# Performance work log

Hardware: AMD Instinct MI355X
Metric: run time of the kernel (lower is better)

Reference implementation:

```python
import jax, jax.numpy as jnp
import numpy as np

B, S, H, NH = 2, 2048, 1024, 16
HD = H // NH  # head_dim = 64


def setup_inputs() -> dict:
    key = jax.random.key(0)
    k1, k2, k3, k4, k5 = jax.random.split(key, 5)
    hidden_states = jax.random.normal(k1, (B, S, H), dtype=jnp.float32)
    # additive causal mask: 0 on/below diagonal, -1e9 above
    causal = jnp.tril(jnp.ones((S, S), dtype=jnp.bool_))
    attention_mask = jnp.where(causal, 0.0, -1e9).astype(jnp.float32)[None, None, :, :]
    scale = 0.02
    Wq = jax.random.normal(k2, (H, H), dtype=jnp.float32) * scale
    Wk = jax.random.normal(k3, (H, H), dtype=jnp.float32) * scale
    Wv = jax.random.normal(k4, (H, H), dtype=jnp.float32) * scale
    Wo = jax.random.normal(k5, (H, H), dtype=jnp.float32) * scale
    return {"hidden_states": hidden_states, "attention_mask": attention_mask,
            "Wq": Wq, "Wk": Wk, "Wv": Wv, "Wo": Wo}


def reference(hidden_states, attention_mask, Wq, Wk, Wv, Wo):
    b, s, _ = hidden_states.shape
    # nn.Linear: y = x @ W.T
    q = (hidden_states @ Wq.T).reshape(b, s, NH, HD).transpose(0, 2, 1, 3)  # [B,NH,S,HD]
    k = (hidden_states @ Wk.T).reshape(b, s, NH, HD).transpose(0, 2, 1, 3)
    v = (hidden_states @ Wv.T).reshape(b, s, NH, HD).transpose(0, 2, 1, 3)
    scores = jnp.einsum('bhqd,bhkd->bhqk', q, k) / jnp.sqrt(jnp.float32(HD))
    scores = scores + attention_mask
    attn = jax.nn.softmax(scores, axis=-1)
    out = jnp.einsum('bhqk,bhkd->bhqd', attn, v)  # [B,NH,S,HD]
    out = out.transpose(0, 2, 1, 3).reshape(b, s, H)
    return out @ Wo.T
```

## Files before the change

### kernel.cpp

```cpp
#include <hip/hip_runtime.h>
#include <hip/hip_bf16.h>

#define B_   2
#define S_   2048
#define H_   1024
#define NH_  16
#define HD_  64
#define MTOT 4096
#define KD   1024

typedef __attribute__((ext_vector_type(4)))  float    f32x4;
typedef __attribute__((ext_vector_type(16))) float    f32x16;
typedef __attribute__((ext_vector_type(8)))  short    bf16x8;
typedef __attribute__((ext_vector_type(4)))  short    bf16x4;
typedef __attribute__((ext_vector_type(2)))  unsigned u32x2;
typedef __attribute__((ext_vector_type(4)))  unsigned u32x4;

__device__ inline short f2bf(float x) {
    union { float f; unsigned u; } v; v.f = x;
    unsigned r = v.u + 0x7fffu + ((v.u >> 16) & 1u);
    return (short)(r >> 16);
}
__device__ inline unsigned pk2(float lo, float hi) {
    return (unsigned)(unsigned short)f2bf(lo) | ((unsigned)(unsigned short)f2bf(hi) << 16);
}
__device__ inline unsigned cvtpk(float lo, float hi) {
    unsigned r;
    asm("v_cvt_pk_bf16_f32 %0, %1, %2" : "=v"(r) : "v"(lo), "v"(hi));
    return r;
}
__device__ inline float max3f(float a, float b, float c) {
    float r;
    asm("v_max3_f32 %0, %1, %2, %3" : "=v"(r) : "v"(a), "v"(b), "v"(c));
    return r;
}
__device__ inline void gload16(const void* g, void* l) {
    __builtin_amdgcn_global_load_lds(
        (const __attribute__((address_space(1))) unsigned*)g,
        (__attribute__((address_space(3))) unsigned*)l, 16, 0, 0);
}

__global__ __launch_bounds__(256) void cvt_x(const float* __restrict__ x,
                                             unsigned* __restrict__ xb) {
    const size_t i = ((size_t)blockIdx.x * 256 + threadIdx.x) * 8;
    const f32x4 a = *(const f32x4*)(x + i);
    const f32x4 b = *(const f32x4*)(x + i + 4);
    u32x4 p;
    p[0] = pk2(a[0], a[1]); p[1] = pk2(a[2], a[3]);
    p[2] = pk2(b[0], b[1]); p[3] = pk2(b[2], b[3]);
    *(u32x4*)(xb + i / 2) = p;
}

__global__ __launch_bounds__(256) void wcvt(const float* __restrict__ W0,
                                            const float* __restrict__ W1,
                                            const float* __restrict__ W2,
                                            const float* __restrict__ W3,
                                            unsigned* __restrict__ wb) {
    const float* W = (blockIdx.y == 0) ? W0 : (blockIdx.y == 1) ? W1
                   : (blockIdx.y == 2) ? W2 : W3;
    const size_t i = ((size_t)blockIdx.x * 256 + threadIdx.x) * 8;
    const f32x4 a = *(const f32x4*)(W + i);
    const f32x4 b = *(const f32x4*)(W + i + 4);
    u32x4 p;
    p[0] = pk2(a[0], a[1]); p[1] = pk2(a[2], a[3]);
    p[2] = pk2(b[0], b[1]); p[3] = pk2(b[2], b[3]);
    *(u32x4*)(wb + (size_t)blockIdx.y * (H_ * KD / 2) + i / 2) = p;
}

template <int MODE>
__global__ __launch_bounds__(256) void gemm_m97(const short* __restrict__ A,
                                                const short* __restrict__ Wb,
                                                short* __restrict__ outb,
                                                float* __restrict__ outf) {
    __shared__ short Sm[128 * 128];
    short* As = Sm;
    short* Bs = Sm + 8192;

    const int tid = threadIdx.x, wave = tid >> 6, lane = tid & 63;
    const int wm = (wave >> 1) * 64, wn = (wave & 1) * 64;
    const int m0 = blockIdx.x * 128;

    int n0, widx;
    if constexpr (MODE == 0) {
        widx = blockIdx.y >> 3;
        n0 = (blockIdx.y & 7) * 128;
    } else {
        widx = 0;
        n0 = blockIdx.y * 128;
    }
    const short* W = Wb + (size_t)widx * H_ * KD;

    f32x4 acc[4][4] = {};

    for (int k0 = 0; k0 < KD; k0 += 64) {
#pragma unroll
        for (int c = 0; c < 4; ++c) {
            const int lin = wave * 4096 + c * 1024 + lane * 16;
            const int row = lin >> 7;
            const int col = (lin & 127) ^ ((row & 7) << 4);
            gload16(A + (size_t)(m0 + row) * KD + k0 + (col >> 1),
                    (char*)As + wave * 4096 + c * 1024);
            gload16(W + (size_t)(n0 + row) * KD + k0 + (col >> 1),
                    (char*)Bs + wave * 4096 + c * 1024);
        }
        __syncthreads();

#pragma unroll
        for (int ks = 0; ks < 2; ++ks) {
            bf16x8 af[4], bf[4];
#pragma unroll
            for (int i = 0; i < 4; ++i) {
                const int row = wm + i * 16 + (lane & 15);
                af[i] = *(const bf16x8*)((char*)As + row * 128 +
                        ((ks * 64 + (lane >> 4) * 16) ^ ((row & 7) << 4)));
            }
#pragma unroll
            for (int j = 0; j < 4; ++j) {
                const int row = wn + j * 16 + (lane & 15);
                bf[j] = *(const bf16x8*)((char*)Bs + row * 128 +
                        ((ks * 64 + (lane >> 4) * 16) ^ ((row & 7) << 4)));
            }
#pragma unroll
            for (int i = 0; i < 4; ++i)
#pragma unroll
                for (int j = 0; j < 4; ++j)
                    acc[i][j] = __builtin_amdgcn_mfma_f32_16x16x32_bf16(af[i], bf[j], acc[i][j], 0, 0, 0);
        }
        __syncthreads();
    }

    if constexpr (MODE == 0) {
        if (widx == 2) {
#pragma unroll
            for (int i = 0; i < 4; ++i)
#pragma unroll
                for (int j = 0; j < 4; ++j) {
                    const int m = m0 + wm + i * 16 + (lane >> 4) * 4;
                    const int n = n0 + wn + j * 16 + (lane & 15);
                    const int bb = m >> 11, s = m & 2047;
                    const int hd = n >> 6, d = n & 63;
                    bf16x4 w;
#pragma unroll
                    for (int r = 0; r < 4; ++r) w[r] = f2bf(acc[i][j][r]);
                    *(bf16x4*)(outb + (size_t)2 * MTOT * H_ +
                               (((size_t)(bb * NH_ + hd)) * HD_ + d) * S_ + s) = w;
                }
        } else {
#pragma unroll
            for (int i = 0; i < 4; ++i)
#pragma unroll
                for (int j = 0; j < 4; ++j)
#pragma unroll
                    for (int r = 0; r < 4; ++r) {
                        const int mi = wm + i * 16 + (lane >> 4) * 4 + r;
                        const int ni = wn + j * 16 + (lane & 15);
                        const int byt = (mi * 256 + ni * 2) ^ ((mi & 7) << 4);
                        *(short*)((char*)Sm + byt) = f2bf(acc[i][j][r]);
                    }
            __syncthreads();
            const int row = tid >> 1, half = tid & 1;
            const int m = m0 + row, bb = m >> 11, s = m & 2047;
            const int hh = (n0 >> 6) + half;
            short* dst = outb + (size_t)widx * MTOT * H_ +
                         (((size_t)(bb * NH_ + hh)) * S_ + s) * HD_;
#pragma unroll
            for (int k = 0; k < 8; ++k) {
                const int byt = (row * 256 + half * 128 + k * 16) ^ ((row & 7) << 4);
                *(bf16x8*)(dst + k * 8) = *(const bf16x8*)((char*)Sm + byt);
            }
        }
    } else {
#pragma unroll
        for (int i = 0; i < 4; ++i)
#pragma unroll
            for (int j = 0; j < 4; ++j)
#pragma unroll
                for (int r = 0; r < 4; ++r) {
                    const int m = m0 + wm + i * 16 + (lane >> 4) * 4 + r;
                    const int n = n0 + wn + j * 16 + (lane & 15);
                    outf[(size_t)m * H_ + n] = acc[i][j][r];
                }
    }
}

__global__ __launch_bounds__(256, 3) void flash5(const short* __restrict__ Qb,
                                                 const short* __restrict__ Kb,
                                                 const short* __restrict__ Vtb,
                                                 short* __restrict__ Ob) {
    const int bx = blockIdx.x;
    const int hi = bx >> 8, u = bx & 255;
    const int h = u >> 4, tq = u & 15;
    const int qt = hi ? (15 - tq) : tq;
    const int b  = hi;

    const int tid = threadIdx.x, qg = tid >> 6, lane = tid & 63;
    const int q0 = qt * 128;
    const int qw0 = q0 + qg * 32;
    const size_t hoff = ((size_t)(b * NH_ + h)) * S_ * HD_;
    const short* Q  = Qb  + hoff;
    const short* K  = Kb  + hoff;
    const short* Vt = Vtb + hoff;

    const int ql = lane & 31;
    const int hh = lane >> 5;

    bf16x8 qf[4];
#pragma unroll
    for (int ds = 0; ds < 4; ++ds)
        qf[ds] = *(const bf16x8*)(Q + (size_t)(qw0 + ql) * HD_ + ds * 16 + hh * 8);

    f32x16 ot[2] = {};
    float mrun = -1e30f, lrun = 0.f;
    const float c2 = 0.18033688011112042f;

    const int niter = (qw0 + 95) >> 6;
    for (int kt = 0; kt < niter; ++kt) {
        bf16x8 kf[2][4];
#pragma unroll
        for (int t = 0; t < 2; ++t)
#pragma unroll
            for (int ds = 0; ds < 4; ++ds)
                kf[t][ds] = *(const bf16x8*)(K + (size_t)(kt * 64 + t * 32 + ql) * HD_ +
                                             ds * 16 + hh * 8);

        f32x16 st[2] = {};
        __builtin_amdgcn_s_setprio(1);
#pragma unroll
        for (int t = 0; t < 2; ++t)
#pragma unroll
            for (int ds = 0; ds < 4; ++ds)
                st[t] = __builtin_amdgcn_mfma_f32_32x32x16_bf16(kf[t][ds], qf[ds], st[t], 0, 0, 0);
        __builtin_amdgcn_s_setprio(0);

        bf16x8 vf[2][4];
#pragma unroll
        for (int dt = 0; dt < 2; ++dt)
#pragma unroll
            for (int ks = 0; ks < 4; ++ks)
                vf[dt][ks] = *(const bf16x8*)(Vt + (size_t)(dt * 32 + ql) * S_ +
                                              kt * 64 + ks * 16 + hh * 8);

        const bool need_mask = (kt * 64 + 63) > qw0;
        float sraw[32];
#pragma unroll
        for (int t = 0; t < 2; ++t)
#pragma unroll
            for (int r = 0; r < 16; ++r) {
                float v = st[t][r];
                if (need_mask) {
                    const int key = kt * 64 + t * 32 + (r & 3) + 8 * (r >> 2) + 4 * hh;
                    if (key > qw0 + ql) v = -1e30f;
                }
                sraw[t * 16 + r] = v;
            }

        float ma = fmaxf(sraw[0], sraw[1]);
        float mb = fmaxf(sraw[2], sraw[3]);
#pragma unroll
        for (int i = 4; i < 32; i += 4) {
            ma = max3f(ma, sraw[i],     sraw[i + 1]);
            mb = max3f(mb, sraw[i + 2], sraw[i + 3]);
        }
        const float pmax = fmaxf(fmaxf(ma, mb), __shfl_xor(fmaxf(ma, mb), 32, 64));

        if (!__all((pmax - mrun) <= 44.36f)) {
            const float mnew = fmaxf(mrun, pmax);
            const float corr = exp2f((mrun - mnew) * c2);
            mrun = mnew;
            lrun *= corr;
#pragma unroll
            for (int dt = 0; dt < 2; ++dt)
#pragma unroll
                for (int r = 0; r < 16; ++r) ot[dt][r] *= corr;
        }
        const float mc = mrun * c2;

        float p[32];
#pragma unroll
        for (int i = 0; i < 32; ++i) p[i] = exp2f(fmaf(sraw[i], c2, -mc));
        float ts[16];
#pragma unroll
        for (int i = 0; i < 16; ++i) ts[i] = p[i] + p[i + 16];
#pragma unroll
        for (int stp = 8; stp >= 1; stp >>= 1)
#pragma unroll
            for (int i = 0; i < 8; ++i)
                if (i < stp) ts[i] += ts[i + stp];
        lrun += ts[0] + __shfl_xor(ts[0], 32, 64);

#pragma unroll
        for (int ks = 0; ks < 4; ++ks) {
            const int t = ks >> 1, rb = (ks & 1) * 8;
            const unsigned a0 = cvtpk(p[t * 16 + rb + 0], p[t * 16 + rb + 1]);
            const unsigned a1 = cvtpk(p[t * 16 + rb + 2], p[t * 16 + rb + 3]);
            const unsigned a2 = cvtpk(p[t * 16 + rb + 4], p[t * 16 + rb + 5]);
            const unsigned a3 = cvtpk(p[t * 16 + rb + 6], p[t * 16 + rb + 7]);
            const unsigned s0 = __shfl_xor(a0, 32, 64);
            const unsigned s1 = __shfl_xor(a1, 32, 64);
            const unsigned s2 = __shfl_xor(a2, 32, 64);
            const unsigned s3 = __shfl_xor(a3, 32, 64);
            u32x4 pw;
            pw[0] = hh ? s2 : a0;
            pw[1] = hh ? s3 : a1;
            pw[2] = hh ? a2 : s0;
            pw[3] = hh ? a3 : s1;
            const bf16x8 pf = __builtin_bit_cast(bf16x8, pw);
            __builtin_amdgcn_s_setprio(1);
#pragma unroll
            for (int dt = 0; dt < 2; ++dt)
                ot[dt] = __builtin_amdgcn_mfma_f32_32x32x16_bf16(vf[dt][ks], pf, ot[dt], 0, 0, 0);
            __builtin_amdgcn_s_setprio(0);
        }
    }

    const float inv = 1.f / lrun;
    short* orow = Ob + ((size_t)(b * S_) + q0 + qg * 32 + ql) * H_ + h * HD_;
#pragma unroll
    for (int dt = 0; dt < 2; ++dt)
#pragma unroll
        for (int g4 = 0; g4 < 4; ++g4) {
            const int dbase = dt * 32 + 8 * g4 + 4 * hh;
            u32x2 w;
            w[0] = cvtpk(ot[dt][g4 * 4 + 0] * inv, ot[dt][g4 * 4 + 1] * inv);
            w[1] = cvtpk(ot[dt][g4 * 4 + 2] * inv, ot[dt][g4 * 4 + 3] * inv);
            *(u32x2*)(orow + dbase) = w;
        }
}

extern "C" void kernel_launch(void* const* d_in, const int* in_sizes, int n_in,
                              void* d_out, int out_size, void* d_ws, size_t ws_size,
                              hipStream_t stream) {
    const float* x  = (const float*)d_in[0];
    const float* Wq = (const float*)d_in[2];
    const float* Wk = (const float*)d_in[3];
    const float* Wv = (const float*)d_in[4];
    const float* Wo = (const float*)d_in[5];
    float* out = (float*)d_out;

    short* qkv = (short*)d_ws;
    short* xb  = qkv + (size_t)3 * MTOT * H_;
    short* wb  = xb + (size_t)MTOT * H_;

    cvt_x<<<2048, 256, 0, stream>>>(x, (unsigned*)xb);
    wcvt<<<dim3(512, 4), 256, 0, stream>>>(Wq, Wk, Wv, Wo, (unsigned*)wb);

    gemm_m97<0><<<dim3(32, 24), 256, 0, stream>>>(xb, wb, qkv, nullptr);

    flash5<<<dim3(512), 256, 0, stream>>>(
        qkv, qkv + (size_t)MTOT * H_, qkv + (size_t)2 * MTOT * H_, xb);

    gemm_m97<1><<<dim3(32, 8), 256, 0, stream>>>(
        xb, wb + (size_t)3 * H_ * KD, nullptr, out);
}
```

Measured before the change: 148.5 us.

## Split KV loop across wave pairs in flash kernel, stage V-transpose stores via LDS

Restructures the flash attention kernel so each wave handles 64 query rows (two 32-row halves sharing K/V fragment loads), and pairs of waves split the key tiles by parity, merging partial softmax states through shared memory at the end. Block-to-(batch, head, query-tile) mapping is changed to pair causal-complementary query tiles within a block and to group heads, for load balance and L2 locality. Separately, the V-transpose epilogue of the QKV GEMM now goes through swizzled LDS to emit 16-byte coalesced stores instead of scattered 8-byte writes. The cost is higher register pressure (launch bounds lowered to 2 blocks per SM), extra LDS, and a final merge step.

```diff
diff --git a/kernel.cpp b/kernel.cpp
--- a/kernel.cpp
+++ b/kernel.cpp
@@ -135,16 +135,24 @@
             for (int i = 0; i < 4; ++i)
 #pragma unroll
                 for (int j = 0; j < 4; ++j) {
-                    const int m = m0 + wm + i * 16 + (lane >> 4) * 4;
-                    const int n = n0 + wn + j * 16 + (lane & 15);
-                    const int bb = m >> 11, s = m & 2047;
-                    const int hd = n >> 6, d = n & 63;
+                    const int mi2 = (wm + i * 16 + (lane >> 4) * 4) * 2;
+                    const int ni  = wn + j * 16 + (lane & 15);
                     bf16x4 w;
 #pragma unroll
                     for (int r = 0; r < 4; ++r) w[r] = f2bf(acc[i][j][r]);
-                    *(bf16x4*)(outb + (size_t)2 * MTOT * H_ +
-                               (((size_t)(bb * NH_ + hd)) * HD_ + d) * S_ + s) = w;
+                    *(bf16x4*)((char*)Sm + ((ni * 256 + mi2) ^ ((ni & 7) << 4))) = w;
                 }
+            __syncthreads();
+            const int d = tid >> 1, shalf = tid & 1;
+            const int bb = m0 >> 11, sbase = (m0 & 2047) + shalf * 64;
+            const int hd = (n0 + d) >> 6, dd = (n0 + d) & 63;
+            short* dst = outb + (size_t)2 * MTOT * H_ +
+                         (((size_t)(bb * NH_ + hd)) * HD_ + dd) * S_ + sbase;
+#pragma unroll
+            for (int k = 0; k < 8; ++k) {
+                const int byt = (d * 256 + shalf * 128 + k * 16) ^ ((d & 7) << 4);
+                *(bf16x8*)(dst + k * 8) = *(const bf16x8*)((char*)Sm + byt);
+            }
         } else {
 #pragma unroll
             for (int i = 0; i < 4; ++i)
@@ -183,19 +191,21 @@
     }
 }
 
-__global__ __launch_bounds__(256, 3) void flash5(const short* __restrict__ Qb,
+__global__ __launch_bounds__(256, 2) void flash6(const short* __restrict__ Qb,
                                                  const short* __restrict__ Kb,
                                                  const short* __restrict__ Vtb,
                                                  short* __restrict__ Ob) {
     const int bx = blockIdx.x;
-    const int hi = bx >> 8, u = bx & 255;
-    const int h = u >> 4, tq = u & 15;
-    const int qt = hi ? (15 - tq) : tq;
-    const int b  = hi;
-
-    const int tid = threadIdx.x, qg = tid >> 6, lane = tid & 63;
-    const int q0 = qt * 128;
-    const int qw0 = q0 + qg * 32;
+    const int x = bx & 7, y = bx >> 3;
+    const int h = x | (((y >> 4) & 1) << 3);
+    const int b = y >> 5;
+    const int j = y & 15;
+
+    const int tid = threadIdx.x, wave = tid >> 6, lane = tid & 63;
+    const int qg = wave >> 1, par = wave & 1;
+    const int qi = qg ? (31 - j) : j;
+    const int qw0 = qi * 64;
+
     const size_t hoff = ((size_t)(b * NH_ + h)) * S_ * HD_;
     const short* Q  = Qb  + hoff;
     const short* K  = Kb  + hoff;
@@ -204,17 +214,19 @@
     const int ql = lane & 31;
     const int hh = lane >> 5;
 
-    bf16x8 qf[4];
-#pragma unroll
-    for (int ds = 0; ds < 4; ++ds)
-        qf[ds] = *(const bf16x8*)(Q + (size_t)(qw0 + ql) * HD_ + ds * 16 + hh * 8);
-
-    f32x16 ot[2] = {};
-    float mrun = -1e30f, lrun = 0.f;
+    bf16x8 qf[2][4];
+#pragma unroll
+    for (int hq = 0; hq < 2; ++hq)
+#pragma unroll
+        for (int ds = 0; ds < 4; ++ds)
+            qf[hq][ds] = *(const bf16x8*)(Q + (size_t)(qw0 + hq * 32 + ql) * HD_ +
+                                          ds * 16 + hh * 8);
+
+    f32x16 ot[2][2] = {};
+    float mrun[2] = {-1e30f, -1e30f}, lrun[2] = {0.f, 0.f};
     const float c2 = 0.18033688011112042f;
 
-    const int niter = (qw0 + 95) >> 6;
-    for (int kt = 0; kt < niter; ++kt) {
+    for (int kt = par; kt <= qi; kt += 2) {
         bf16x8 kf[2][4];
 #pragma unroll
         for (int t = 0; t < 2; ++t)
@@ -223,13 +235,15 @@
                 kf[t][ds] = *(const bf16x8*)(K + (size_t)(kt * 64 + t * 32 + ql) * HD_ +
                                              ds * 16 + hh * 8);
 
-        f32x16 st[2] = {};
+        f32x16 st[2][2] = {};
         __builtin_amdgcn_s_setprio(1);
 #pragma unroll
-        for (int t = 0; t < 2; ++t)
-#pragma unroll
-            for (int ds = 0; ds < 4; ++ds)
-                st[t] = __builtin_amdgcn_mfma_f32_32x32x16_bf16(kf[t][ds], qf[ds], st[t], 0, 0, 0);
+        for (int hq = 0; hq < 2; ++hq)
+#pragma unroll
+            for (int t = 0; t < 2; ++t)
+#pragma unroll
+                for (int ds = 0; ds < 4; ++ds)
+                    st[hq][t] = __builtin_amdgcn_mfma_f32_32x32x16_bf16(kf[t][ds], qf[hq][ds], st[hq][t], 0, 0, 0);
         __builtin_amdgcn_s_setprio(0);
 
         bf16x8 vf[2][4];
@@ -240,91 +254,133 @@
                 vf[dt][ks] = *(const bf16x8*)(Vt + (size_t)(dt * 32 + ql) * S_ +
                                               kt * 64 + ks * 16 + hh * 8);
 
-        const bool need_mask = (kt * 64 + 63) > qw0;
-        float sraw[32];
-#pragma unroll
-        for (int t = 0; t < 2; ++t)
-#pragma unroll
-            for (int r = 0; r < 16; ++r) {
-                float v = st[t][r];
-                if (need_mask) {
-                    const int key = kt * 64 + t * 32 + (r & 3) + 8 * (r >> 2) + 4 * hh;
-                    if (key > qw0 + ql) v = -1e30f;
+        const bool nm = (kt == qi);
+        u32x4 pa[2][4];
+#pragma unroll
+        for (int hq = 0; hq < 2; ++hq) {
+            const int qrow = qw0 + hq * 32 + ql;
+            float sraw[32];
+#pragma unroll
+            for (int t = 0; t < 2; ++t)
+#pragma unroll
+                for (int r = 0; r < 16; ++r) {
+                    float v = st[hq][t][r];
+                    if (nm) {
+                        const int key = kt * 64 + t * 32 + (r & 3) + 8 * (r >> 2) + 4 * hh;
+                        if (key > qrow) v = -1e30f;
+                    }
+                    sraw[t * 16 + r] = v;
                 }
-                sraw[t * 16 + r] = v;
-            }
-
-        float ma = fmaxf(sraw[0], sraw[1]);
-        float mb = fmaxf(sraw[2], sraw[3]);
-#pragma unroll
-        for (int i = 4; i < 32; i += 4) {
-            ma = max3f(ma, sraw[i],     sraw[i + 1]);
-            mb = max3f(mb, sraw[i + 2], sraw[i + 3]);
+
+            float ma = fmaxf(sraw[0], sraw[1]);
+            float mb = fmaxf(sraw[2], sraw[3]);
+#pragma unroll
+            for (int i = 4; i < 32; i += 4) {
+                ma = max3f(ma, sraw[i],     sraw[i + 1]);
+                mb = max3f(mb, sraw[i + 2], sraw[i + 3]);
+            }
+            const float pmax = fmaxf(fmaxf(ma, mb), __shfl_xor(fmaxf(ma, mb), 32, 64));
+
+            if (!__all((pmax - mrun[hq]) <= 44.36f)) {
+                const float mnew = fmaxf(mrun[hq], pmax);
+                const float corr = exp2f((mrun[hq] - mnew) * c2);
+                mrun[hq] = mnew;
+                lrun[hq] *= corr;
+#pragma unroll
+                for (int dt = 0; dt < 2; ++dt)
+#pragma unroll
+                    for (int r = 0; r < 16; ++r) ot[hq][dt][r] *= corr;
+            }
+            const float mc = mrun[hq] * c2;
+
+            float p[32];
+#pragma unroll
+            for (int i = 0; i < 32; ++i) p[i] = exp2f(fmaf(sraw[i], c2, -mc));
+            float ts[16];
+#pragma unroll
+            for (int i = 0; i < 16; ++i) ts[i] = p[i] + p[i + 16];
+#pragma unroll
+            for (int stp = 8; stp >= 1; stp >>= 1)
+#pragma unroll
+                for (int i = 0; i < 8; ++i)
+                    if (i < stp) ts[i] += ts[i + stp];
+            lrun[hq] += ts[0] + __shfl_xor(ts[0], 32, 64);
+
+#pragma unroll
+            for (int ks = 0; ks < 4; ++ks) {
+                const int t = ks >> 1, rb = (ks & 1) * 8;
+                const unsigned a0 = cvtpk(p[t * 16 + rb + 0], p[t * 16 + rb + 1]);
+                const unsigned a1 = cvtpk(p[t * 16 + rb + 2], p[t * 16 + rb + 3]);
+                const unsigned a2 = cvtpk(p[t * 16 + rb + 4], p[t * 16 + rb + 5]);
+                const unsigned a3 = cvtpk(p[t * 16 + rb + 6], p[t * 16 + rb + 7]);
+                const unsigned s0 = __shfl_xor(a0, 32, 64);
+                const unsigned s1 = __shfl_xor(a1, 32, 64);
+                const unsigned s2 = __shfl_xor(a2, 32, 64);
+                const unsigned s3 = __shfl_xor(a3, 32, 64);
+                u32x4 pw;
+                pw[0] = hh ? s2 : a0;
+                pw[1] = hh ? s3 : a1;
+                pw[2] = hh ? a2 : s0;
+                pw[3] = hh ? a3 : s1;
+                pa[hq][ks] = pw;
+            }
         }
-        const float pmax = fmaxf(fmaxf(ma, mb), __shfl_xor(fmaxf(ma, mb), 32, 64));
-
-        if (!__all((pmax - mrun) <= 44.36f)) {
-            const float mnew = fmaxf(mrun, pmax);
-            const float corr = exp2f((mrun - mnew) * c2);
-            mrun = mnew;
-            lrun *= corr;
+
+        __builtin_amdgcn_s_setprio(1);
+#pragma unroll
+        for (int ks = 0; ks < 4; ++ks)
 #pragma unroll
             for (int dt = 0; dt < 2; ++dt)
 #pragma unroll
-                for (int r = 0; r < 16; ++r) ot[dt][r] *= corr;
+                for (int hq = 0; hq < 2; ++hq)
+                    ot[hq][dt] = __builtin_amdgcn_mfma_f32_32x32x16_bf16(
+                        vf[dt][ks], __builtin_bit_cast(bf16x8, pa[hq][ks]), ot[hq][dt], 0, 0, 0);
+        __builtin_amdgcn_s_setprio(0);
+    }
+
+    __shared__ float Osh[2][64][66];
+    __shared__ float Msh[2][64][4];
+
+    if (par == 1) {
+#pragma unroll
+        for (int hq = 0; hq < 2; ++hq)
+#pragma unroll
+            for (int dt = 0; dt < 2; ++dt)
+#pragma unroll
+                for (int r = 0; r < 16; ++r)
+                    Osh[qg][lane][hq * 32 + dt * 16 + r] = ot[hq][dt][r];
+        Msh[qg][lane][0] = mrun[0]; Msh[qg][lane][1] = lrun[0];
+        Msh[qg][lane][2] = mrun[1]; Msh[qg][lane][3] = lrun[1];
+    }
+    __syncthreads();
+
+    if (par == 0) {
+#pragma unroll
+        for (int hq = 0; hq < 2; ++hq) {
+            const float mB = Msh[qg][lane][hq * 2 + 0];
+            const float lB = Msh[qg][lane][hq * 2 + 1];
+            const float m  = fmaxf(mrun[hq], mB);
+            const float al = exp2f((mrun[hq] - m) * c2);
+            const float be = exp2f((mB - m) * c2);
+            const float inv = 1.f / (al * lrun[hq] + be * lB);
+            const float ai = al * inv, bi = be * inv;
+
+            short* orow = Ob + ((size_t)(b * S_) + qw0 + hq * 32 + ql) * H_ + h * HD_;
+#pragma unroll
+            for (int dt = 0; dt < 2; ++dt)
+#pragma unroll
+                for (int g4 = 0; g4 < 4; ++g4) {
+                    const int base = hq * 32 + dt * 16 + g4 * 4;
+                    const int dbase = dt * 32 + 8 * g4 + 4 * hh;
+                    u32x2 w;
+                    w[0] = cvtpk(ot[hq][dt][g4 * 4 + 0] * ai + Osh[qg][lane][base + 0] * bi,
+                                 ot[hq][dt][g4 * 4 + 1] * ai + Osh[qg][lane][base + 1] * bi);
+                    w[1] = cvtpk(ot[hq][dt][g4 * 4 + 2] * ai + Osh[qg][lane][base + 2] * bi,
+                                 ot[hq][dt][g4 * 4 + 3] * ai + Osh[qg][lane][base + 3] * bi);
+                    *(u32x2*)(orow + dbase) = w;
+                }
         }
-        const float mc = mrun * c2;
-
-        float p[32];
-#pragma unroll
-        for (int i = 0; i < 32; ++i) p[i] = exp2f(fmaf(sraw[i], c2, -mc));
-        float ts[16];
-#pragma unroll
-        for (int i = 0; i < 16; ++i) ts[i] = p[i] + p[i + 16];
-#pragma unroll
-        for (int stp = 8; stp >= 1; stp >>= 1)
-#pragma unroll
-            for (int i = 0; i < 8; ++i)
-                if (i < stp) ts[i] += ts[i + stp];
-        lrun += ts[0] + __shfl_xor(ts[0], 32, 64);
-
-#pragma unroll
-        for (int ks = 0; ks < 4; ++ks) {
-            const int t = ks >> 1, rb = (ks & 1) * 8;
-            const unsigned a0 = cvtpk(p[t * 16 + rb + 0], p[t * 16 + rb + 1]);
-            const unsigned a1 = cvtpk(p[t * 16 + rb + 2], p[t * 16 + rb + 3]);
-            const unsigned a2 = cvtpk(p[t * 16 + rb + 4], p[t * 16 + rb + 5]);
-            const unsigned a3 = cvtpk(p[t * 16 + rb + 6], p[t * 16 + rb + 7]);
-            const unsigned s0 = __shfl_xor(a0, 32, 64);
-            const unsigned s1 = __shfl_xor(a1, 32, 64);
-            const unsigned s2 = __shfl_xor(a2, 32, 64);
-            const unsigned s3 = __shfl_xor(a3, 32, 64);
-            u32x4 pw;
-            pw[0] = hh ? s2 : a0;
-            pw[1] = hh ? s3 : a1;
-            pw[2] = hh ? a2 : s0;
-            pw[3] = hh ? a3 : s1;
-            const bf16x8 pf = __builtin_bit_cast(bf16x8, pw);
-            __builtin_amdgcn_s_setprio(1);
-#pragma unroll
-            for (int dt = 0; dt < 2; ++dt)
-                ot[dt] = __builtin_amdgcn_mfma_f32_32x32x16_bf16(vf[dt][ks], pf, ot[dt], 0, 0, 0);
-            __builtin_amdgcn_s_setprio(0);
-        }
-    }
-
-    const float inv = 1.f / lrun;
-    short* orow = Ob + ((size_t)(b * S_) + q0 + qg * 32 + ql) * H_ + h * HD_;
-#pragma unroll
-    for (int dt = 0; dt < 2; ++dt)
-#pragma unroll
-        for (int g4 = 0; g4 < 4; ++g4) {
-            const int dbase = dt * 32 + 8 * g4 + 4 * hh;
-            u32x2 w;
-            w[0] = cvtpk(ot[dt][g4 * 4 + 0] * inv, ot[dt][g4 * 4 + 1] * inv);
-            w[1] = cvtpk(ot[dt][g4 * 4 + 2] * inv, ot[dt][g4 * 4 + 3] * inv);
-            *(u32x2*)(orow + dbase) = w;
-        }
+    }
 }
 
 extern "C" void kernel_launch(void* const* d_in, const int* in_sizes, int n_in,
@@ -346,7 +402,7 @@
 
     gemm_m97<0><<<dim3(32, 24), 256, 0, stream>>>(xb, wb, qkv, nullptr);
 
-    flash5<<<dim3(512), 256, 0, stream>>>(
+    flash6<<<dim3(512), 256, 0, stream>>>(
         qkv, qkv + (size_t)MTOT * H_, qkv + (size_t)2 * MTOT * H_, xb);
 
     gemm_m97<1><<<dim3(32, 8), 256, 0, stream>>>(
```

Measured after the change: 162.3 us. 9.3% more time.

## Split attention KV loop across waves and stage V transpose through LDS

Applied to the files above, without the earlier changes.

The flash kernel now gives each block a single 32-query tile, and its four waves each take every fourth KV tile. Partial outputs, running maxima and sums are then merged through shared memory with rescaling, and wave 0 writes the result. The grid grows fourfold, heaviest tiles first, with higher occupancy bounds. This targets causal load imbalance and poor parallelism, at the cost of a serialized LDS reduction and more K/V traffic. Separately, the V-transpose store in the QKV GEMM now goes through swizzled LDS so global writes are coalesced 16-byte rows instead of scattered 8-byte ones.

```diff
diff --git a/kernel.cpp b/kernel.cpp
--- a/kernel.cpp
+++ b/kernel.cpp
@@ -135,16 +135,24 @@
             for (int i = 0; i < 4; ++i)
 #pragma unroll
                 for (int j = 0; j < 4; ++j) {
-                    const int m = m0 + wm + i * 16 + (lane >> 4) * 4;
-                    const int n = n0 + wn + j * 16 + (lane & 15);
-                    const int bb = m >> 11, s = m & 2047;
-                    const int hd = n >> 6, d = n & 63;
+                    const int mi2 = (wm + i * 16 + (lane >> 4) * 4) * 2;
+                    const int ni  = wn + j * 16 + (lane & 15);
                     bf16x4 w;
 #pragma unroll
                     for (int r = 0; r < 4; ++r) w[r] = f2bf(acc[i][j][r]);
-                    *(bf16x4*)(outb + (size_t)2 * MTOT * H_ +
-                               (((size_t)(bb * NH_ + hd)) * HD_ + d) * S_ + s) = w;
+                    *(bf16x4*)((char*)Sm + ((ni * 256 + mi2) ^ ((ni & 7) << 4))) = w;
                 }
+            __syncthreads();
+            const int d = tid >> 1, shalf = tid & 1;
+            const int bb = m0 >> 11, sbase = (m0 & 2047) + shalf * 64;
+            const int hd = (n0 + d) >> 6, dd = (n0 + d) & 63;
+            short* dst = outb + (size_t)2 * MTOT * H_ +
+                         (((size_t)(bb * NH_ + hd)) * HD_ + dd) * S_ + sbase;
+#pragma unroll
+            for (int k = 0; k < 8; ++k) {
+                const int byt = (d * 256 + shalf * 128 + k * 16) ^ ((d & 7) << 4);
+                *(bf16x8*)(dst + k * 8) = *(const bf16x8*)((char*)Sm + byt);
+            }
         } else {
 #pragma unroll
             for (int i = 0; i < 4; ++i)
@@ -183,19 +191,17 @@
     }
 }
 
-__global__ __launch_bounds__(256, 3) void flash5(const short* __restrict__ Qb,
+__global__ __launch_bounds__(256, 4) void flash7(const short* __restrict__ Qb,
                                                  const short* __restrict__ Kb,
                                                  const short* __restrict__ Vtb,
                                                  short* __restrict__ Ob) {
     const int bx = blockIdx.x;
-    const int hi = bx >> 8, u = bx & 255;
-    const int h = u >> 4, tq = u & 15;
-    const int qt = hi ? (15 - tq) : tq;
-    const int b  = hi;
-
-    const int tid = threadIdx.x, qg = tid >> 6, lane = tid & 63;
-    const int q0 = qt * 128;
-    const int qw0 = q0 + qg * 32;
+    const int qu = 63 - (bx >> 5);
+    const int bh = bx & 31;
+    const int b = bh >> 4, h = bh & 15;
+
+    const int tid = threadIdx.x, par = tid >> 6, lane = tid & 63;
+    const int qw0 = qu * 32;
     const size_t hoff = ((size_t)(b * NH_ + h)) * S_ * HD_;
     const short* Q  = Qb  + hoff;
     const short* K  = Kb  + hoff;
@@ -214,7 +220,7 @@
     const float c2 = 0.18033688011112042f;
 
     const int niter = (qw0 + 95) >> 6;
-    for (int kt = 0; kt < niter; ++kt) {
+    for (int kt = par; kt < niter; kt += 4) {
         bf16x8 kf[2][4];
 #pragma unroll
         for (int t = 0; t < 2; ++t)
@@ -313,18 +319,60 @@
         }
     }
 
-    const float inv = 1.f / lrun;
-    short* orow = Ob + ((size_t)(b * S_) + q0 + qg * 32 + ql) * H_ + h * HD_;
-#pragma unroll
-    for (int dt = 0; dt < 2; ++dt)
-#pragma unroll
-        for (int g4 = 0; g4 < 4; ++g4) {
-            const int dbase = dt * 32 + 8 * g4 + 4 * hh;
-            u32x2 w;
-            w[0] = cvtpk(ot[dt][g4 * 4 + 0] * inv, ot[dt][g4 * 4 + 1] * inv);
-            w[1] = cvtpk(ot[dt][g4 * 4 + 2] * inv, ot[dt][g4 * 4 + 3] * inv);
-            *(u32x2*)(orow + dbase) = w;
-        }
+    __shared__ float Osh[64][36];
+    __shared__ float Msh[64][2];
+
+#pragma unroll 1
+    for (int r = 1; r < 4; ++r) {
+        if (par == r) {
+#pragma unroll
+            for (int dt = 0; dt < 2; ++dt)
+#pragma unroll
+                for (int g4 = 0; g4 < 4; ++g4) {
+                    f32x4 t;
+                    t[0] = ot[dt][g4 * 4 + 0]; t[1] = ot[dt][g4 * 4 + 1];
+                    t[2] = ot[dt][g4 * 4 + 2]; t[3] = ot[dt][g4 * 4 + 3];
+                    *(f32x4*)(&Osh[lane][dt * 16 + g4 * 4]) = t;
+                }
+            Msh[lane][0] = mrun;
+            Msh[lane][1] = lrun;
+        }
+        __syncthreads();
+        if (par == 0) {
+            const float mB = Msh[lane][0];
+            const float lB = Msh[lane][1];
+            const float m  = fmaxf(mrun, mB);
+            const float al = exp2f((mrun - m) * c2);
+            const float be = exp2f((mB - m) * c2);
+#pragma unroll
+            for (int dt = 0; dt < 2; ++dt)
+#pragma unroll
+                for (int g4 = 0; g4 < 4; ++g4) {
+                    const f32x4 ob = *(const f32x4*)(&Osh[lane][dt * 16 + g4 * 4]);
+#pragma unroll
+                    for (int rr = 0; rr < 4; ++rr)
+                        ot[dt][g4 * 4 + rr] = ot[dt][g4 * 4 + rr] * al + ob[rr] * be;
+                }
+            lrun = lrun * al + lB * be;
+            mrun = m;
+        }
+        __syncthreads();
+    }
+
+    if (par == 0) {
+        const float inv = 1.f / lrun;
+        short* orow = Ob + ((size_t)(b * S_) + qw0 + ql) * H_ + h * HD_;
+#pragma unroll
+        for (int dt = 0; dt < 2; ++dt)
+#pragma unroll
+            for (int g4 = 0; g4 < 4; ++g4) {
+                const int dbase = dt * 32 + 8 * g4 + 4 * hh;
+                u32x2 w;
+                w[0] = cvtpk(ot[dt][g4 * 4 + 0] * inv, ot[dt][g4 * 4 + 1] * inv);
+                w[1] = cvtpk(ot[dt][g4 * 4 + 2] * inv, ot[dt][g4 * 4 + 3] * inv);
+                *(u32x2*)(orow + dbase) = w;
+            }
+    }
 }
 
 extern "C" void kernel_launch(void* const* d_in, const int* in_sizes, int n_in,
@@ -346,7 +394,7 @@
 
     gemm_m97<0><<<dim3(32, 24), 256, 0, stream>>>(xb, wb, qkv, nullptr);
 
-    flash5<<<dim3(512), 256, 0, stream>>>(
+    flash7<<<dim3(2048), 256, 0, stream>>>(
         qkv, qkv + (size_t)MTOT * H_, qkv + (size_t)2 * MTOT * H_, xb);
 
     gemm_m97<1><<<dim3(32, 8), 256, 0, stream>>>(
```

New measurement: 187.0 us. +26.0%, slower.
